# Performance work log

Measured on AMD Instinct MI355X. Metric: run time of the kernel, lower is better.

Reference implementation:

```python
import jax, jax.numpy as jnp
import numpy as np

B, S, D, H = 4, 2048, 1024, 16
HD = D // H  # head dim = 64


def setup_inputs() -> dict:
    key = jax.random.key(0)
    ks = jax.random.split(key, 12)
    scale = 0.02
    inp = {
        "query": jax.random.normal(ks[0], (B, S, D), jnp.float32),
        "key": jax.random.normal(ks[1], (B, S, D), jnp.float32),
        "value": jax.random.normal(ks[2], (B, S, D), jnp.float32),
        "mask": jax.random.randint(ks[3], (B, 1, 1, S), 0, 2, jnp.int32),
        "wq": scale * jax.random.normal(ks[4], (D, D), jnp.float32),
        "bq": jnp.zeros((D,), jnp.float32),
        "wk": scale * jax.random.normal(ks[5], (D, D), jnp.float32),
        "bk": jnp.zeros((D,), jnp.float32),
        "wv": scale * jax.random.normal(ks[6], (D, D), jnp.float32),
        "bv": jnp.zeros((D,), jnp.float32),
        "wo": scale * jax.random.normal(ks[7], (D, D), jnp.float32),
        "bo": jnp.zeros((D,), jnp.float32),
    }
    return inp


def reference(query, key, value, mask, wq, bq, wk, bk, wv, bv, wo, bo):
    # Linear projections (torch Linear: x @ W^T + b)
    Q = (query @ wq.T + bq).reshape(B, S, H, HD).transpose(0, 2, 1, 3)  # [B,H,S,HD]
    K = (key @ wk.T + bk).reshape(B, S, H, HD).transpose(0, 2, 1, 3)    # [B,H,S,HD]
    V = (value @ wv.T + bv).reshape(B, S, H, HD).transpose(0, 2, 1, 3)  # [B,H,S,HD]

    inv_sqrt_d = jnp.asarray(1.0 / np.sqrt(HD), Q.dtype)
    score = jnp.einsum("bhqd,bhkd->bhqk", Q, K) * inv_sqrt_d  # [B,H,S,S]
    score = jnp.where(mask == 0, jnp.asarray(-1e9, score.dtype), score)
    weights = jax.nn.softmax(score, axis=-1)  # dropout p=0 -> identity (eval)
    attn = jnp.einsum("bhqk,bhkd->bhqd", weights, V)  # [B,H,S,HD]
    attn = attn.transpose(0, 2, 1, 3).reshape(B, S, D)
    return attn @ wo.T + bo
```

## Files before the change

kernel.cpp:

```cpp
#include <hip/hip_runtime.h>
#include <hip/hip_bf16.h>
#include <stdint.h>


typedef __bf16 bh;
typedef bh bh8 __attribute__((ext_vector_type(8)));
typedef float f4 __attribute__((ext_vector_type(4)));

#define DEVI static __device__ __forceinline__

constexpr int CB = 4, CS = 2048, CD = 1024, CH = 16;
constexpr int CM = CB * CS;

DEVI f4 mfma16(bh8 a, bh8 b, f4 c) {
  return __builtin_amdgcn_mfma_f32_16x16x32_bf16(a, b, c, 0, 0, 0);
}

DEVI void gload_lds16(const void* g, void* l) {
  void* gnc = const_cast<void*>(g);
  __builtin_amdgcn_global_load_lds(
      (__attribute__((address_space(1))) void*)gnc,
      (__attribute__((address_space(3))) void*)l, 16, 0, 0);
}

DEVI bh8 frag_ld(const bh* base, int row, int k0) {
  int slot = (k0 >> 3) ^ (row & 7);
  return *(const bh8*)(base + row * 64 + slot * 8);
}

DEVI bh8 frag_ld2(const bh* base, int row, int k0) {
  int slot = ((k0 >> 3) ^ (row & 7) ^ ((row >> 3) & 7)) & 7;
  return *(const bh8*)(base + row * 64 + slot * 8);
}

DEVI bh8 cvt8(float4 a, float4 b) {
  bh8 v;
  v[0] = (bh)a.x; v[1] = (bh)a.y; v[2] = (bh)a.z; v[3] = (bh)a.w;
  v[4] = (bh)b.x; v[5] = (bh)b.y; v[6] = (bh)b.z; v[7] = (bh)b.w;
  return v;
}

__global__ void cast_kern(const float* __restrict__ in, bh* __restrict__ out,
                          int n) {
  int i = (blockIdx.x * 256 + threadIdx.x) * 8;
  if (i < n) {
    const float4* p = (const float4*)(in + i);
    *(bh8*)(out + i) = cvt8(p[0], p[1]);
  }
}

DEVI void stage_bf16_tile(const bh* src, int ld, bh* dst, int wave, int lane) {
#pragma unroll
  for (int i = 0; i < 4; ++i) {
    int c = i * 256 + wave * 64 + lane;
    int row = c >> 3, s8 = c & 7;
    gload_lds16(src + (size_t)row * ld + ((s8 ^ (row & 7)) * 8), dst + c * 8);
  }
}

template <bool OUT_F32>
__global__ __launch_bounds__(256, 2) void gemm_bt(
    const bh* __restrict__ Ap, const bh* __restrict__ Bw,
    const float* __restrict__ bias, void* __restrict__ Cp,
    int M, int N, int K) {
  __shared__ __align__(16) bh Asm[128 * 64];
  __shared__ __align__(16) bh Bsm[128 * 64];
  const int t = threadIdx.x;
  const int lane = t & 63, wave = t >> 6;
  const int wm = wave >> 1, wn = wave & 1;

  const int ntx = N >> 7, nty = M >> 7;
  const int c = blockIdx.x & 7;
  const int l = blockIdx.x >> 3;
  const int mt = c * (nty >> 3) + l / ntx;
  const int nt = l % ntx;
  const int m0 = mt * 128, n0 = nt * 128;
  const int r15 = lane & 15, g4 = lane >> 4;

  const f4 fz = {0.f, 0.f, 0.f, 0.f};
  f4 acc[4][4];
#pragma unroll
  for (int i = 0; i < 4; ++i)
#pragma unroll
    for (int j = 0; j < 4; ++j) acc[i][j] = fz;

  for (int kt = 0; kt < K; kt += 64) {
    stage_bf16_tile(Ap + (size_t)m0 * K + kt, K, Asm, wave, lane);
    stage_bf16_tile(Bw + (size_t)n0 * K + kt, K, Bsm, wave, lane);
    __syncthreads();

    bh8 af[4][2], bf_[4][2];
#pragma unroll
    for (int m = 0; m < 4; ++m)
#pragma unroll
      for (int kk = 0; kk < 2; ++kk)
        af[m][kk] = frag_ld(Asm, wm * 64 + m * 16 + r15, kk * 32 + g4 * 8);
#pragma unroll
    for (int n = 0; n < 4; ++n)
#pragma unroll
      for (int kk = 0; kk < 2; ++kk)
        bf_[n][kk] = frag_ld(Bsm, wn * 64 + n * 16 + r15, kk * 32 + g4 * 8);
#pragma unroll
    for (int kk = 0; kk < 2; ++kk)
#pragma unroll
      for (int m = 0; m < 4; ++m)
#pragma unroll
        for (int n = 0; n < 4; ++n)
          acc[m][n] = mfma16(af[m][kk], bf_[n][kk], acc[m][n]);
    __syncthreads();
  }

#pragma unroll
  for (int n = 0; n < 4; ++n) {
    int col = n0 + wn * 64 + n * 16 + r15;
    float bv = bias[col];
#pragma unroll
    for (int m = 0; m < 4; ++m) {
      int row = m0 + wm * 64 + m * 16 + g4 * 4;
#pragma unroll
      for (int r = 0; r < 4; ++r) {
        float v = acc[m][n][r] + bv;
        if constexpr (OUT_F32)
          ((float*)Cp)[(size_t)(row + r) * N + col] = v;
        else
          ((bh*)Cp)[(size_t)(row + r) * N + col] = (bh)v;
      }
    }
  }
}

__global__ __launch_bounds__(256, 2) void attn_fwd(
    const bh* __restrict__ Qp, const bh* __restrict__ Kp,
    const bh* __restrict__ Vp, const int* __restrict__ maskp,
    bh* __restrict__ Op) {
  __shared__ __align__(16) bh Ksm[64 * 64];
  __shared__ __align__(16) bh Vtsm[64 * 64];
  __shared__ __align__(16) bh Psm[64 * 64];
  __shared__ float maskadd[64];

  const int t = threadIdx.x;
  const int lane = t & 63, wave = t >> 6;
  const int r15 = lane & 15, g4 = lane >> 4;
  const int b = blockIdx.y >> 4, h = blockIdx.y & 15;
  const int q0 = blockIdx.x * 64;

  const bh* Qb = Qp + ((size_t)(b * CS + q0)) * CD + h * 64;
  const bh* Kb = Kp + ((size_t)b * CS) * CD + h * 64;
  const bh* Vb = Vp + ((size_t)b * CS) * CD + h * 64;
  const int* mb = maskp + b * CS;

  bh8 qf[2];
  {
    int qr = wave * 16 + r15;
#pragma unroll
    for (int kk = 0; kk < 2; ++kk) {
      bh8 v = *(const bh8*)(Qb + (size_t)qr * CD + kk * 32 + g4 * 8);
#pragma unroll
      for (int j = 0; j < 8; ++j) v[j] = (bh)((float)v[j] * 0.125f);
      qf[kk] = v;
    }
  }

  const f4 fz = {0.f, 0.f, 0.f, 0.f};
  f4 acc_o[4];
#pragma unroll
  for (int i = 0; i < 4; ++i) acc_o[i] = fz;
  float mrow[4] = {-1e30f, -1e30f, -1e30f, -1e30f};
  float lrow[4] = {0.f, 0.f, 0.f, 0.f};

  for (int kt = 0; kt < CS; kt += 64) {
    const bh* Ks = Kb + (size_t)kt * CD;
#pragma unroll
    for (int i = 0; i < 2; ++i) {
      int c = i * 256 + wave * 64 + lane;
      int row = c >> 3, s8 = c & 7;
      gload_lds16(Ks + (size_t)row * CD + ((s8 ^ (row & 7)) * 8), Ksm + c * 8);
    }
    const bh* Vs = Vb + (size_t)kt * CD;
#pragma unroll
    for (int i = 0; i < 2; ++i) {
      int c = i * 256 + t;
      int k = c >> 3, d0 = (c & 7) * 8;
      bh8 v = *(const bh8*)(Vs + (size_t)k * CD + d0);
#pragma unroll
      for (int j = 0; j < 8; ++j) {
        int dr = d0 + j;
        int slot = ((k >> 3) ^ (dr & 7) ^ ((dr >> 3) & 7)) & 7;
        Vtsm[dr * 64 + slot * 8 + (k & 7)] = v[j];
      }
    }
    if (t < 64) maskadd[t] = (mb[kt + t] == 0) ? -1e9f : 0.0f;
    __syncthreads();

    f4 s[4];
#pragma unroll
    for (int tt = 0; tt < 4; ++tt) {
      f4 a = fz;
#pragma unroll
      for (int kk = 0; kk < 2; ++kk) {
        bh8 kf = frag_ld(Ksm, tt * 16 + r15, kk * 32 + g4 * 8);
        a = mfma16(qf[kk], kf, a);
      }
      s[tt] = a;
    }

    float madd[4];
#pragma unroll
    for (int tt = 0; tt < 4; ++tt) madd[tt] = maskadd[tt * 16 + r15];
    float mx[4];
#pragma unroll
    for (int r = 0; r < 4; ++r) {
      float v0 = s[0][r] + madd[0];
      s[0][r] = v0;
      mx[r] = v0;
    }
#pragma unroll
    for (int tt = 1; tt < 4; ++tt)
#pragma unroll
      for (int r = 0; r < 4; ++r) {
        float v = s[tt][r] + madd[tt];
        s[tt][r] = v;
        mx[r] = fmaxf(mx[r], v);
      }
#pragma unroll
    for (int off = 1; off < 16; off <<= 1)
#pragma unroll
      for (int r = 0; r < 4; ++r) mx[r] = fmaxf(mx[r], __shfl_xor(mx[r], off));

    float corr[4];
#pragma unroll
    for (int r = 0; r < 4; ++r) {
      float mn = fmaxf(mrow[r], mx[r]);
      corr[r] = __expf(mrow[r] - mn);
      mrow[r] = mn;
    }
    float psum[4];
#pragma unroll
    for (int tt = 0; tt < 4; ++tt)
#pragma unroll
      for (int r = 0; r < 4; ++r) {
        float p = __expf(s[tt][r] - mrow[r]);
        s[tt][r] = p;
        psum[r] = (tt == 0) ? p : (psum[r] + p);
      }
#pragma unroll
    for (int off = 1; off < 16; off <<= 1)
#pragma unroll
      for (int r = 0; r < 4; ++r) psum[r] += __shfl_xor(psum[r], off);
#pragma unroll
    for (int r = 0; r < 4; ++r) lrow[r] = lrow[r] * corr[r] + psum[r];
#pragma unroll
    for (int tt = 0; tt < 4; ++tt)
#pragma unroll
      for (int r = 0; r < 4; ++r) acc_o[tt][r] *= corr[r];

#pragma unroll
    for (int tt = 0; tt < 4; ++tt)
#pragma unroll
      for (int r = 0; r < 4; ++r) {
        int row = wave * 16 + g4 * 4 + r;
        int col = tt * 16 + r15;
        int slot = ((col >> 3) ^ (row & 7) ^ ((row >> 3) & 7)) & 7;
        Psm[row * 64 + slot * 8 + (col & 7)] = (bh)s[tt][r];
      }

    bh8 pf[2];
#pragma unroll
    for (int kk = 0; kk < 2; ++kk)
      pf[kk] = frag_ld2(Psm, wave * 16 + r15, kk * 32 + g4 * 8);
#pragma unroll
    for (int tt = 0; tt < 4; ++tt)
#pragma unroll
      for (int kk = 0; kk < 2; ++kk) {
        bh8 vf = frag_ld2(Vtsm, tt * 16 + r15, kk * 32 + g4 * 8);
        acc_o[tt] = mfma16(pf[kk], vf, acc_o[tt]);
      }
    __syncthreads();
  }

  bh* Ob = Op + ((size_t)(b * CS + q0)) * CD + h * 64;
#pragma unroll
  for (int tt = 0; tt < 4; ++tt)
#pragma unroll
    for (int r = 0; r < 4; ++r) {
      int row = wave * 16 + g4 * 4 + r;
      int col = tt * 16 + r15;
      Ob[(size_t)row * CD + col] = (bh)(acc_o[tt][r] / lrow[r]);
    }
}

extern "C" void kernel_launch(void* const* d_in, const int* in_sizes, int n_in,
                              void* d_out, int out_size, void* d_ws,
                              size_t ws_size, hipStream_t stream) {
  const float* query = (const float*)d_in[0];
  const float* key   = (const float*)d_in[1];
  const float* value = (const float*)d_in[2];
  const int*   mask  = (const int*)d_in[3];
  const float* wq = (const float*)d_in[4];
  const float* bq = (const float*)d_in[5];
  const float* wk = (const float*)d_in[6];
  const float* bk = (const float*)d_in[7];
  const float* wv = (const float*)d_in[8];
  const float* bv = (const float*)d_in[9];
  const float* wo = (const float*)d_in[10];
  const float* bo = (const float*)d_in[11];
  float* out = (float*)d_out;

  const size_t TN = (size_t)CM * CD;
  bh* Qp = (bh*)d_ws;
  bh* Kp = Qp + TN;
  bh* Vp = Kp + TN;
  bh* Ap = Vp + TN;
  bh* Xbf = (bh*)d_out;
  bh* Wbf = Xbf + TN;
  bh* Wlate = Qp;

  const int nW = CD * CD;
  const int wB = nW / (256 * 8);
  const int nX = CM * CD;
  const int xB = nX / (256 * 8);
  const int nwg = (CD / 128) * (CM / 128);

  cast_kern<<<wB, 256, 0, stream>>>(wq, Wbf, nW);
  cast_kern<<<xB, 256, 0, stream>>>(query, Xbf, nX);
  gemm_bt<false><<<nwg, 256, 0, stream>>>(Xbf, Wbf, bq, Qp, CM, CD, CD);
  cast_kern<<<wB, 256, 0, stream>>>(wk, Wbf, nW);
  cast_kern<<<xB, 256, 0, stream>>>(key, Xbf, nX);
  gemm_bt<false><<<nwg, 256, 0, stream>>>(Xbf, Wbf, bk, Kp, CM, CD, CD);
  cast_kern<<<wB, 256, 0, stream>>>(wv, Wbf, nW);
  cast_kern<<<xB, 256, 0, stream>>>(value, Xbf, nX);
  gemm_bt<false><<<nwg, 256, 0, stream>>>(Xbf, Wbf, bv, Vp, CM, CD, CD);
  attn_fwd<<<dim3(CS / 64, CB * CH), 256, 0, stream>>>(Qp, Kp, Vp, mask, Ap);
  cast_kern<<<wB, 256, 0, stream>>>(wo, Wlate, nW);
  gemm_bt<true><<<nwg, 256, 0, stream>>>(Ap, Wlate, bo, out, CM, CD, CD);
}
```

Before: 520.3 us.

## Transpose QK MFMA so softmax rows live per lane, pack LDS stores

```diff
diff --git a/kernel.cpp b/kernel.cpp
--- a/kernel.cpp
+++ b/kernel.cpp
@@ -4,8 +4,11 @@
 
 
 typedef __bf16 bh;
+typedef bh bh4 __attribute__((ext_vector_type(4)));
 typedef bh bh8 __attribute__((ext_vector_type(8)));
 typedef float f4 __attribute__((ext_vector_type(4)));
+typedef unsigned u32;
+typedef u32 u32x2 __attribute__((ext_vector_type(2)));
 
 #define DEVI static __device__ __forceinline__
 
@@ -32,6 +35,13 @@
   int slot = ((k0 >> 3) ^ (row & 7) ^ ((row >> 3) & 7)) & 7;
   return *(const bh8*)(base + row * 64 + slot * 8);
 }
+
+DEVI u32 pkbb(bh a, bh b) {
+  unsigned short ua = __builtin_bit_cast(unsigned short, a);
+  unsigned short ub = __builtin_bit_cast(unsigned short, b);
+  return (u32)ua | ((u32)ub << 16);
+}
+DEVI u32 pkff(float a, float b) { return pkbb((bh)a, (bh)b); }
 
 DEVI bh8 cvt8(float4 a, float4 b) {
   bh8 v;
@@ -136,7 +146,6 @@
   __shared__ __align__(16) bh Ksm[64 * 64];
   __shared__ __align__(16) bh Vtsm[64 * 64];
   __shared__ __align__(16) bh Psm[64 * 64];
-  __shared__ float maskadd[64];
 
   const int t = threadIdx.x;
   const int lane = t & 63, wave = t >> 6;
@@ -165,8 +174,10 @@
   f4 acc_o[4];
 #pragma unroll
   for (int i = 0; i < 4; ++i) acc_o[i] = fz;
-  float mrow[4] = {-1e30f, -1e30f, -1e30f, -1e30f};
-  float lrow[4] = {0.f, 0.f, 0.f, 0.f};
+  float mrow = -1e30f, lrow = 0.f;
+
+  const int vk0 = (t >> 4) * 4;
+  const int vd0 = (t & 15) * 4;
 
   for (int kt = 0; kt < CS; kt += 64) {
     const bh* Ks = Kb + (size_t)kt * CD;
@@ -176,20 +187,22 @@
       int row = c >> 3, s8 = c & 7;
       gload_lds16(Ks + (size_t)row * CD + ((s8 ^ (row & 7)) * 8), Ksm + c * 8);
     }
-    const bh* Vs = Vb + (size_t)kt * CD;
-#pragma unroll
-    for (int i = 0; i < 2; ++i) {
-      int c = i * 256 + t;
-      int k = c >> 3, d0 = (c & 7) * 8;
-      bh8 v = *(const bh8*)(Vs + (size_t)k * CD + d0);
-#pragma unroll
-      for (int j = 0; j < 8; ++j) {
-        int dr = d0 + j;
-        int slot = ((k >> 3) ^ (dr & 7) ^ ((dr >> 3) & 7)) & 7;
-        Vtsm[dr * 64 + slot * 8 + (k & 7)] = v[j];
-      }
-    }
-    if (t < 64) maskadd[t] = (mb[kt + t] == 0) ? -1e9f : 0.0f;
+    {
+      const bh* Vs = Vb + (size_t)kt * CD;
+      bh4 vl[4];
+#pragma unroll
+      for (int i = 0; i < 4; ++i)
+        vl[i] = *(const bh4*)(Vs + (size_t)(vk0 + i) * CD + vd0);
+#pragma unroll
+      for (int i = 0; i < 4; ++i) {
+        int d = vd0 + i;
+        u32x2 w2;
+        w2[0] = pkbb(vl[0][i], vl[1][i]);
+        w2[1] = pkbb(vl[2][i], vl[3][i]);
+        int slot = ((vk0 >> 3) ^ (d & 7) ^ ((d >> 3) & 7)) & 7;
+        *(u32x2*)(Vtsm + d * 64 + slot * 8 + (vk0 & 7)) = w2;
+      }
+    }
     __syncthreads();
 
     f4 s[4];
@@ -199,75 +212,69 @@
 #pragma unroll
       for (int kk = 0; kk < 2; ++kk) {
         bh8 kf = frag_ld(Ksm, tt * 16 + r15, kk * 32 + g4 * 8);
-        a = mfma16(qf[kk], kf, a);
+        a = mfma16(kf, qf[kk], a);
       }
       s[tt] = a;
     }
 
-    float madd[4];
-#pragma unroll
-    for (int tt = 0; tt < 4; ++tt) madd[tt] = maskadd[tt * 16 + r15];
-    float mx[4];
-#pragma unroll
-    for (int r = 0; r < 4; ++r) {
-      float v0 = s[0][r] + madd[0];
-      s[0][r] = v0;
-      mx[r] = v0;
-    }
-#pragma unroll
-    for (int tt = 1; tt < 4; ++tt)
+#pragma unroll
+    for (int tt = 0; tt < 4; ++tt) {
+      int4 mv = *(const int4*)(mb + kt + tt * 16 + 4 * g4);
+      s[tt][0] += (mv.x == 0) ? -1e9f : 0.0f;
+      s[tt][1] += (mv.y == 0) ? -1e9f : 0.0f;
+      s[tt][2] += (mv.z == 0) ? -1e9f : 0.0f;
+      s[tt][3] += (mv.w == 0) ? -1e9f : 0.0f;
+    }
+
+    float pm = s[0][0];
+#pragma unroll
+    for (int tt = 0; tt < 4; ++tt)
+#pragma unroll
+      for (int r = 0; r < 4; ++r) pm = fmaxf(pm, s[tt][r]);
+    pm = fmaxf(pm, __shfl_xor(pm, 16));
+    pm = fmaxf(pm, __shfl_xor(pm, 32));
+
+    float mn = fmaxf(mrow, pm);
+    float corr = __expf(mrow - mn);
+    mrow = mn;
+    float psum = 0.f;
+#pragma unroll
+    for (int tt = 0; tt < 4; ++tt)
 #pragma unroll
       for (int r = 0; r < 4; ++r) {
-        float v = s[tt][r] + madd[tt];
-        s[tt][r] = v;
-        mx[r] = fmaxf(mx[r], v);
-      }
-#pragma unroll
-    for (int off = 1; off < 16; off <<= 1)
-#pragma unroll
-      for (int r = 0; r < 4; ++r) mx[r] = fmaxf(mx[r], __shfl_xor(mx[r], off));
-
-    float corr[4];
-#pragma unroll
-    for (int r = 0; r < 4; ++r) {
-      float mn = fmaxf(mrow[r], mx[r]);
-      corr[r] = __expf(mrow[r] - mn);
-      mrow[r] = mn;
-    }
-    float psum[4];
+        float p = __expf(s[tt][r] - mn);
+        s[tt][r] = p;
+        psum += p;
+      }
+    psum += __shfl_xor(psum, 16);
+    psum += __shfl_xor(psum, 32);
+    lrow = lrow * corr + psum;
+
+    float co[4];
+#pragma unroll
+    for (int r = 0; r < 4; ++r) co[r] = __shfl(corr, 4 * g4 + r);
 #pragma unroll
     for (int tt = 0; tt < 4; ++tt)
 #pragma unroll
-      for (int r = 0; r < 4; ++r) {
-        float p = __expf(s[tt][r] - mrow[r]);
-        s[tt][r] = p;
-        psum[r] = (tt == 0) ? p : (psum[r] + p);
-      }
-#pragma unroll
-    for (int off = 1; off < 16; off <<= 1)
-#pragma unroll
-      for (int r = 0; r < 4; ++r) psum[r] += __shfl_xor(psum[r], off);
-#pragma unroll
-    for (int r = 0; r < 4; ++r) lrow[r] = lrow[r] * corr[r] + psum[r];
-#pragma unroll
-    for (int tt = 0; tt < 4; ++tt)
-#pragma unroll
-      for (int r = 0; r < 4; ++r) acc_o[tt][r] *= corr[r];
-
-#pragma unroll
-    for (int tt = 0; tt < 4; ++tt)
-#pragma unroll
-      for (int r = 0; r < 4; ++r) {
-        int row = wave * 16 + g4 * 4 + r;
-        int col = tt * 16 + r15;
-        int slot = ((col >> 3) ^ (row & 7) ^ ((row >> 3) & 7)) & 7;
-        Psm[row * 64 + slot * 8 + (col & 7)] = (bh)s[tt][r];
-      }
+      for (int r = 0; r < 4; ++r) acc_o[tt][r] *= co[r];
+
+    {
+      int q = wave * 16 + r15;
+#pragma unroll
+      for (int tt = 0; tt < 4; ++tt) {
+        int key0 = tt * 16 + 4 * g4;
+        u32x2 w2;
+        w2[0] = pkff(s[tt][0], s[tt][1]);
+        w2[1] = pkff(s[tt][2], s[tt][3]);
+        int slot = ((key0 >> 3) ^ (q & 7)) & 7;
+        *(u32x2*)(Psm + q * 64 + slot * 8 + (key0 & 7)) = w2;
+      }
+    }
 
     bh8 pf[2];
 #pragma unroll
     for (int kk = 0; kk < 2; ++kk)
-      pf[kk] = frag_ld2(Psm, wave * 16 + r15, kk * 32 + g4 * 8);
+      pf[kk] = frag_ld(Psm, wave * 16 + r15, kk * 32 + g4 * 8);
 #pragma unroll
     for (int tt = 0; tt < 4; ++tt)
 #pragma unroll
@@ -278,6 +285,9 @@
     __syncthreads();
   }
 
+  float lo[4];
+#pragma unroll
+  for (int r = 0; r < 4; ++r) lo[r] = __shfl(lrow, 4 * g4 + r);
   bh* Ob = Op + ((size_t)(b * CS + q0)) * CD + h * 64;
 #pragma unroll
   for (int tt = 0; tt < 4; ++tt)
@@ -285,7 +295,7 @@
     for (int r = 0; r < 4; ++r) {
       int row = wave * 16 + g4 * 4 + r;
       int col = tt * 16 + r15;
-      Ob[(size_t)row * CD + col] = (bh)(acc_o[tt][r] / lrow[r]);
+      Ob[(size_t)row * CD + col] = (bh)(acc_o[tt][r] / lo[r]);
     }
 }
 
```

Result: faster. 440.2 us (-15.4%).
